# Optimization experiments

Hardware: AMD Instinct MI355X
Metric: run time of the kernel (lower is better)

## Reference

```python
import jax, jax.numpy as jnp
import numpy as np

V = 100000   # nodes
E = 1600000  # edges (avg degree 16)
LN = 64      # feat_dim
S = 8        # stat_dim
T = 4        # recurrence steps
MU = 0.9
N_EDGE_TYPES = 10


def _uniform_linear(kw, kb, fan_out, fan_in):
    # torch nn.Linear default init: U(-1/sqrt(fan_in), 1/sqrt(fan_in))
    lim = 1.0 / np.sqrt(fan_in)
    W = jax.random.uniform(kw, (fan_out, fan_in), jnp.float32, -lim, lim)
    b = jax.random.uniform(kb, (fan_out,), jnp.float32, -lim, lim)
    return W, b


def setup_inputs() -> dict:
    key = jax.random.key(0)
    ks = jax.random.split(key, 12)
    feat_Matrix = jax.random.normal(ks[0], (V, LN), jnp.float32)
    X_Node = jax.random.randint(ks[1], (E,), 1, V + 1, dtype=jnp.int64)   # 1-indexed
    X_Neis = jax.random.randint(ks[2], (E,), 1, V + 1, dtype=jnp.int64)   # 1-indexed
    edge_type_index = jax.random.randint(ks[3], (E,), 1, N_EDGE_TYPES + 1, dtype=jnp.int32)
    dg_list = jax.random.randint(ks[4], (E,), 1, 65).astype(jnp.float32)  # degrees >= 1
    H_init = jax.random.uniform(ks[5], (V, S), jnp.float32)  # torch.rand init of state
    W_xi, b_xi = _uniform_linear(ks[6], ks[7], S * S, 2 * LN + N_EDGE_TYPES)
    W_rou, b_rou = _uniform_linear(ks[8], ks[9], S, LN)
    W1, b1 = _uniform_linear(ks[10], ks[11], 1, S)
    return {
        "feat_Matrix": feat_Matrix, "X_Node": X_Node, "X_Neis": X_Neis,
        "edge_type_index": edge_type_index, "dg_list": dg_list, "H_init": H_init,
        "W_xi": W_xi, "b_xi": b_xi, "W_rou": W_rou, "b_rou": b_rou,
        "W1": W1, "b1": b1,
    }


def reference(feat_Matrix, X_Node, X_Neis, edge_type_index, dg_list, H_init,
              W_xi, b_xi, W_rou, b_rou, W1, b1):
    src = X_Node - 1           # 0-indexed source nodes
    dst = X_Neis - 1           # 0-indexed neighbor nodes (for embedding gather)
    node_emb = feat_Matrix[src]            # [E, LN]
    neis_emb = feat_Matrix[dst]            # [E, LN]
    et = jax.nn.one_hot(edge_type_index - 1, N_EDGE_TYPES, dtype=jnp.float32)
    X = jnp.concatenate([node_emb, neis_emb, et], axis=1)  # [E, 2*LN+10]

    # Xi(X): per-edge transition matrices A, constant across steps -> precompute
    A = jnp.tanh(X @ W_xi.T + b_xi).reshape(-1, S, S)
    A = A * (MU / S) / dg_list[:, None, None]              # [E, S, S]
    # Rou(neis_emb): per-edge bias b, constant across steps
    bias = jnp.tanh(neis_emb @ W_rou.T + b_rou)            # [E, S]

    def step(H, _):
        He = H[src]                                        # gather [E, S]
        out = jnp.einsum('eij,ej->ei', A, He) + bias       # per-edge small matmul
        # AggrSum: dense one-hot mask vs RAW 1-indexed X_Neis against range(0,V-1)
        # -> scatter by 1-indexed ids; ids == V fall out of range and are dropped.
        Hn = jax.ops.segment_sum(out, X_Neis, num_segments=V)
        return Hn, None

    H, _ = jax.lax.scan(step, H_init, None, length=T)      # [V, S]

    logits = (H @ W1.T + b1).squeeze(-1)                   # [V]
    attn = jax.nn.softmax(logits)                          # softmax over nodes
    graph_out = jnp.tanh(jnp.sum(H * attn[:, None], axis=0))  # [S]
    return graph_out
```

## Files before the change

### kernel.cpp

```cpp
#include <hip/hip_runtime.h>
#include <hip/hip_bf16.h>

constexpr int V   = 100000;
constexpr int E   = 1600000;
constexpr int NET = 10;
constexpr int KXW = 138;
constexpr int NB  = (V + 255) / 256;
constexpr int GN  = 8;
constexpr int NEB = E / 256;
constexpr int NPQ = (V / 16 + 3) / 4;
constexpr float MUS   = 0.1125f;
constexpr float SP    = 0.025f;
constexpr float LOG2E = 1.44269504f;
constexpr float S2L   = 2.0f * SP * LOG2E;
constexpr float K7    = MUS / 7.0f;

typedef __attribute__((ext_vector_type(8))) short short8;
typedef __attribute__((ext_vector_type(4))) float float4v;

__device__ __forceinline__ float fast_tanh(float x) {
    return 1.0f - 2.0f * __builtin_amdgcn_rcpf(__expf(2.0f * x) + 1.0f);
}
__device__ __forceinline__ float bflo(unsigned u) { return __uint_as_float(u << 16); }
__device__ __forceinline__ float bfhi(unsigned u) { return __uint_as_float(u & 0xffff0000u); }
__device__ __forceinline__ short f2bf(float x) {
    union { __hip_bfloat16 b; short s; } u; u.b = __float2bfloat16(x); return u.s;
}

__device__ __forceinline__ float ub0(unsigned u) {
#if __has_builtin(__builtin_amdgcn_cvt_f32_ubyte0)
    return __builtin_amdgcn_cvt_f32_ubyte0(u);
#else
    return (float)(u & 0xff);
#endif
}
__device__ __forceinline__ float ub1(unsigned u) {
#if __has_builtin(__builtin_amdgcn_cvt_f32_ubyte1)
    return __builtin_amdgcn_cvt_f32_ubyte1(u);
#else
    return (float)((u >> 8) & 0xff);
#endif
}
__device__ __forceinline__ float ub2(unsigned u) {
#if __has_builtin(__builtin_amdgcn_cvt_f32_ubyte2)
    return __builtin_amdgcn_cvt_f32_ubyte2(u);
#else
    return (float)((u >> 16) & 0xff);
#endif
}
__device__ __forceinline__ float ub3(unsigned u) {
#if __has_builtin(__builtin_amdgcn_cvt_f32_ubyte3)
    return __builtin_amdgcn_cvt_f32_ubyte3(u);
#else
    return (float)(u >> 24);
#endif
}

__device__ __forceinline__ int dot8i4(unsigned a, unsigned b, int c) {
#if __has_builtin(__builtin_amdgcn_sdot8)
    return __builtin_amdgcn_sdot8((int)a, (int)b, c, false);
#else
    int r = c;
    #pragma unroll
    for (int j = 0; j < 8; ++j) {
        int av = ((int)(a << (28 - 4 * j))) >> 28;
        int bv = ((int)(b << (28 - 4 * j))) >> 28;
        r += av * bv;
    }
    return r;
#endif
}

__global__ __launch_bounds__(256) void histg_pq_kernel(
    const int* __restrict__ xneis, int* __restrict__ countg,
    int* __restrict__ rank0,
    const float* __restrict__ feat, const float* __restrict__ Wxi,
    unsigned char* __restrict__ P8, ushort* __restrict__ Qb)
{
    if (blockIdx.x < NEB) {
        int e = blockIdx.x * 256 + threadIdx.x;
        int g = blockIdx.x & (GN - 1);
        int nr = xneis[e];
        if (nr < V) rank0[e] = atomicAdd(&countg[g * V + nr], 1);
        return;
    }
    int bid = blockIdx.x - NEB;
    const int lane = threadIdx.x & 63, wave = threadIdx.x >> 6;
    const int quad = lane >> 4, l16 = lane & 15;

    short8 bP[4][2], bQ[4][2];
    #pragma unroll
    for (int nt = 0; nt < 4; ++nt) {
        #pragma unroll
        for (int ks = 0; ks < 2; ++ks) {
            const float* wp = Wxi + (size_t)(nt * 16 + l16) * KXW + ks * 32 + quad * 8;
            short8 p, q;
            #pragma unroll
            for (int j = 0; j < 8; ++j) { p[j] = f2bf(wp[j]); q[j] = f2bf(wp[64 + j]); }
            bP[nt][ks] = p; bQ[nt][ks] = q;
        }
    }

    int t = bid * 4 + wave;
    if (t >= V / 16) return;
    int v0 = t * 16;

    const float* fp = feat + (size_t)(v0 + l16) * 64 + quad * 8;
    short8 a0, a1;
    #pragma unroll
    for (int j = 0; j < 8; ++j) { a0[j] = f2bf(fp[j]); a1[j] = f2bf(fp[32 + j]); }

    float4v accP[4], accQ[4];
    #pragma unroll
    for (int nt = 0; nt < 4; ++nt) {
        float4v z = {0.f, 0.f, 0.f, 0.f};
        z = __builtin_amdgcn_mfma_f32_16x16x32_bf16(a0, bP[nt][0], z, 0, 0, 0);
        z = __builtin_amdgcn_mfma_f32_16x16x32_bf16(a1, bP[nt][1], z, 0, 0, 0);
        accP[nt] = z;
        float4v w = {0.f, 0.f, 0.f, 0.f};
        w = __builtin_amdgcn_mfma_f32_16x16x32_bf16(a0, bQ[nt][0], w, 0, 0, 0);
        w = __builtin_amdgcn_mfma_f32_16x16x32_bf16(a1, bQ[nt][1], w, 0, 0, 0);
        accQ[nt] = w;
    }

    #pragma unroll
    for (int r = 0; r < 4; ++r) {
        int row = v0 + quad * 4 + r;
        #pragma unroll
        for (int nt = 0; nt < 4; ++nt) {
            int col = nt * 16 + l16;
            int q8 = (int)rintf(accP[nt][r] * (1.0f / SP)) + 128;
            q8 = min(max(q8, 0), 255);
            P8[row * 64 + col] = (unsigned char)q8;
            Qb[row * 64 + col] = (ushort)f2bf(accQ[nt][r]);
        }
    }
}

__global__ __launch_bounds__(256) void scanV_bsum_kernel(
    const int* __restrict__ countg, int* __restrict__ offg,
    int* __restrict__ scanned, int* __restrict__ bsumT,
    const float* __restrict__ feat, const float* __restrict__ Wrou,
    const float* __restrict__ brou, const float* __restrict__ Hinit,
    float* __restrict__ Bsum, uint2* __restrict__ Hq0)
{
    __shared__ int s[256];
    __shared__ float Wl[512];
    __shared__ float bl[8];
    int tid = threadIdx.x;
    for (int i = tid; i < 512; i += 256) Wl[i] = Wrou[i];
    if (tid < 8) bl[tid] = brou[tid];

    int v = blockIdx.x * 256 + tid;
    int c = 0;
    if (v < V) {
        int run = 0;
        #pragma unroll
        for (int g = 0; g < GN; ++g) {
            offg[g * V + v] = run;
            run += countg[g * V + v];
        }
        c = run;
    }
    s[tid] = c; __syncthreads();
    #pragma unroll
    for (int off = 1; off < 256; off <<= 1) {
        int t = (tid >= off) ? s[tid - off] : 0;
        __syncthreads();
        s[tid] += t;
        __syncthreads();
    }
    if (v < V) scanned[v] = s[tid] - c;
    if (tid == 255) bsumT[blockIdx.x] = s[255];

    if (v >= V) return;
    float out[8] = {0, 0, 0, 0, 0, 0, 0, 0};
    if (c > 0) {
        const float4* f4 = (const float4*)(feat + (size_t)(v - 1) * 64);
        float acc[8];
        #pragma unroll
        for (int ss = 0; ss < 8; ++ss) acc[ss] = bl[ss];
        #pragma unroll 4
        for (int k = 0; k < 16; ++k) {
            float4 x = f4[k];
            #pragma unroll
            for (int ss = 0; ss < 8; ++ss) {
                const float* w = &Wl[ss * 64 + k * 4];
                acc[ss] += x.x * w[0] + x.y * w[1] + x.z * w[2] + x.w * w[3];
            }
        }
        float fc = (float)c;
        #pragma unroll
        for (int ss = 0; ss < 8; ++ss) out[ss] = fc * fast_tanh(acc[ss]);
    }
    float4* O = (float4*)(Bsum + (size_t)v * 8);
    O[0] = make_float4(out[0], out[1], out[2], out[3]);
    O[1] = make_float4(out[4], out[5], out[6], out[7]);

    const float4* Hh4 = (const float4*)(Hinit + (size_t)v * 8);
    float4 h0 = Hh4[0], h1 = Hh4[1];
    float hv[8] = {h0.x, h0.y, h0.z, h0.w, h1.x, h1.y, h1.z, h1.w};
    float mx = 0.0f;
    #pragma unroll
    for (int i = 0; i < 8; ++i) mx = fmaxf(mx, fabsf(hv[i]));
    float si = (mx > 0.0f) ? 7.0f / mx : 0.0f;
    unsigned w = 0;
    #pragma unroll
    for (int i = 0; i < 8; ++i)
        w |= ((unsigned)((int)rintf(hv[i] * si)) & 0xFu) << (4 * i);
    Hq0[v] = make_uint2(w, __float_as_uint(mx * (1.0f / 7.0f)));
}

__global__ __launch_bounds__(512) void scan_tops_kernel(
    const int* __restrict__ blocksum, int* __restrict__ tops, int* __restrict__ rowptr)
{
    __shared__ int s[512];
    int tid = threadIdx.x;
    int v = (tid < NB) ? blocksum[tid] : 0;
    s[tid] = v; __syncthreads();
    #pragma unroll
    for (int off = 1; off < 512; off <<= 1) {
        int t = (tid >= off) ? s[tid - off] : 0;
        __syncthreads();
        s[tid] += t;
        __syncthreads();
    }
    if (tid < NB) tops[tid] = s[tid] - v;
    if (tid == 511) rowptr[V] = s[511];
}

__global__ __launch_bounds__(256) void add_offsets_kernel(
    const int* __restrict__ scanned, const int* __restrict__ tops, int* __restrict__ rowptr)
{
    int i = blockIdx.x * 256 + threadIdx.x;
    if (i < V) rowptr[i] = scanned[i] + tops[blockIdx.x];
}

__global__ __launch_bounds__(256) void scatterA_kernel(
    const int* __restrict__ xnode, const int* __restrict__ xneis,
    const int* __restrict__ etype, const float* __restrict__ dg,
    const int* __restrict__ rowptr, const int* __restrict__ offg,
    const int* __restrict__ rank0, uint2* __restrict__ buc,
    int* __restrict__ bcnt)
{
    __shared__ int wcnt[4][8];
    __shared__ int woff[4][8];
    int tid = threadIdx.x;
    int lane = tid & 63, wv = tid >> 6;
    int e = blockIdx.x * 256 + tid;
    int g = blockIdx.x & (GN - 1);

    int nr = xneis[e];
    bool keep = (nr < V);
    int p = -1, r = 0;
    if (keep) {
        p = rowptr[nr] + offg[g * V + nr] + rank0[e];
        r = p >> 18;
    }

    unsigned rnk = 0;
    #pragma unroll
    for (int r8 = 0; r8 < 8; ++r8) {
        unsigned long long m = __ballot(keep && (r == r8));
        if (keep && r == r8)
            rnk = (unsigned)__popcll(m & ((1ull << lane) - 1ull));
        if (lane == 0) wcnt[wv][r8] = (int)__popcll(m);
    }
    __syncthreads();
    if (tid < 8) {
        int run = 0;
        #pragma unroll
        for (int w = 0; w < 4; ++w) { woff[w][tid] = run; run += wcnt[w][tid]; }
        bcnt[blockIdx.x * 8 + tid] = run;
    }
    __syncthreads();

    if (keep) {
        unsigned src = (unsigned)(xnode[e] - 1);
        unsigned et  = (unsigned)(etype[e] - 1);
        unsigned dgi = (unsigned)dg[e] - 1;
        unsigned meta = src | (et << 17) | (dgi << 21);
        int slot = blockIdx.x * 2048 + r * 256 + woff[wv][r] + (int)rnk;
        buc[slot] = make_uint2((unsigned)p, meta);
    }
}

__global__ __launch_bounds__(256) void drain_kernel(
    const uint2* __restrict__ buc, const int* __restrict__ bcnt,
    unsigned* __restrict__ pmeta)
{
    int r = blockIdx.x & 7;
    int nstride = (int)(gridDim.x >> 3);
    for (int sb = (int)(blockIdx.x >> 3); sb < NEB; sb += nstride) {
        int c = bcnt[sb * 8 + r];
        const uint2* seg = buc + (size_t)sb * 2048 + r * 256;
        for (int i = threadIdx.x; i < c; i += 256) {
            uint2 t = seg[i];
            pmeta[t.x] = t.y;
        }
    }
}

__global__ __launch_bounds__(256) void amat_kernel(
    const unsigned* __restrict__ pmeta, const int* __restrict__ rowptr,
    const unsigned char* __restrict__ P8, const ushort* __restrict__ Qb,
    const float* __restrict__ Wxi, const float* __restrict__ bxi,
    const uint2* __restrict__ Hq0, const float* __restrict__ Bsum,
    unsigned* __restrict__ A4, uint2* __restrict__ HqOut)
{
    __shared__ float Wet2[NET * 64];
    int tid = threadIdx.x;
    for (int i = tid; i < NET * 64; i += 256) {
        int et = i >> 6, n = i & 63;
        Wet2[i] = 2.0f * LOG2E * (Wxi[n * KXW + 128 + et] + bxi[n]);
    }
    __syncthreads();

    int v = blockIdx.x * 4 + (tid >> 6);
    if (v >= V) return;
    int lane = tid & 63;
    int el = lane >> 3, s = lane & 7;

    const int off = rowptr[v];
    const int deg = rowptr[v + 1] - off;

    float q0, q1, q2, q3, q4, q5, q6, q7;
    {
        uint4 qu = *(const uint4*)(Qb + v * 64 + s * 8);
        const float B = 128.0f * SP, C = 2.0f * LOG2E;
        q0 = C * (bflo(qu.x) - B); q1 = C * (bfhi(qu.x) - B);
        q2 = C * (bflo(qu.y) - B); q3 = C * (bfhi(qu.y) - B);
        q4 = C * (bflo(qu.z) - B); q5 = C * (bfhi(qu.z) - B);
        q6 = C * (bflo(qu.w) - B); q7 = C * (bfhi(qu.w) - B);
    }

    float accD = 0.0f;

    for (int base = 0; base < deg; base += 64) {
        unsigned m_mine = 0;
        {
            int i1 = base + lane;
            if (i1 < deg) m_mine = pmeta[off + i1];
        }
        int nb = deg - base;
        for (int k = 0; k * 8 + el < nb && k < 8; ++k) {
            int ib = k * 8 + el;
            int i = base + ib;
            unsigned m = __shfl(m_mine, ib);
            int src = (int)(m & 0x1FFFF);
            int et  = (int)((m >> 17) & 0xF);

            uint2 pu = *(const uint2*)(P8 + src * 64 + s * 8);
            const float4* w4 = (const float4*)(&Wet2[et * 64 + s * 8]);
            float4 wa = w4[0], wb = w4[1];
            uint2 hq = Hq0[src];

            float r0 = __builtin_amdgcn_rcpf(__builtin_amdgcn_exp2f(fmaf(ub0(pu.x), S2L, q0 + wa.x)) + 1.0f);
            float r1 = __builtin_amdgcn_rcpf(__builtin_amdgcn_exp2f(fmaf(ub1(pu.x), S2L, q1 + wa.y)) + 1.0f);
            float r2 = __builtin_amdgcn_rcpf(__builtin_amdgcn_exp2f(fmaf(ub2(pu.x), S2L, q2 + wa.z)) + 1.0f);
            float r3 = __builtin_amdgcn_rcpf(__builtin_amdgcn_exp2f(fmaf(ub3(pu.x), S2L, q3 + wa.w)) + 1.0f);
            float r4 = __builtin_amdgcn_rcpf(__builtin_amdgcn_exp2f(fmaf(ub0(pu.y), S2L, q4 + wb.x)) + 1.0f);
            float r5 = __builtin_amdgcn_rcpf(__builtin_amdgcn_exp2f(fmaf(ub1(pu.y), S2L, q5 + wb.y)) + 1.0f);
            float r6 = __builtin_amdgcn_rcpf(__builtin_amdgcn_exp2f(fmaf(ub2(pu.y), S2L, q6 + wb.z)) + 1.0f);
            float r7 = __builtin_amdgcn_rcpf(__builtin_amdgcn_exp2f(fmaf(ub3(pu.y), S2L, q7 + wb.w)) + 1.0f);

            int n0 = (int)rintf(fmaf(r0, -14.0f, 7.0f));
            int n1 = (int)rintf(fmaf(r1, -14.0f, 7.0f));
            int n2 = (int)rintf(fmaf(r2, -14.0f, 7.0f));
            int n3 = (int)rintf(fmaf(r3, -14.0f, 7.0f));
            int n4 = (int)rintf(fmaf(r4, -14.0f, 7.0f));
            int n5 = (int)rintf(fmaf(r5, -14.0f, 7.0f));
            int n6 = (int)rintf(fmaf(r6, -14.0f, 7.0f));
            int n7 = (int)rintf(fmaf(r7, -14.0f, 7.0f));

            unsigned w = ((unsigned)n0 & 0xFu)        | (((unsigned)n1 & 0xFu) << 4)
                       | (((unsigned)n2 & 0xFu) << 8)  | (((unsigned)n3 & 0xFu) << 12)
                       | (((unsigned)n4 & 0xFu) << 16) | (((unsigned)n5 & 0xFu) << 20)
                       | (((unsigned)n6 & 0xFu) << 24) | (((unsigned)n7 & 0xFu) << 28);
            A4[(unsigned)(off + i) * 8u + (unsigned)s] = w;

            int dd = dot8i4(w, hq.x, 0);
            float rdg = __builtin_amdgcn_rcpf((float)((int)(m >> 21) + 1));
            accD = fmaf((float)dd, __uint_as_float(hq.y) * rdg, accD);
        }
    }
    accD += __shfl_xor(accD, 8);  accD += __shfl_xor(accD, 16); accD += __shfl_xor(accD, 32);
    float h1v = accD * K7 + Bsum[v * 8 + s];

    float mx = fabsf(h1v);
    mx = fmaxf(mx, __shfl_xor(mx, 1));
    mx = fmaxf(mx, __shfl_xor(mx, 2));
    mx = fmaxf(mx, __shfl_xor(mx, 4));
    float si = (mx > 0.0f) ? 7.0f / mx : 0.0f;
    unsigned nib = (unsigned)((int)rintf(h1v * si)) & 0xFu;
    unsigned b1 = __shfl(nib, lane + 1), b2 = __shfl(nib, lane + 2), b3 = __shfl(nib, lane + 3);
    unsigned b4 = __shfl(nib, lane + 4), b5 = __shfl(nib, lane + 5);
    unsigned b6 = __shfl(nib, lane + 6), b7 = __shfl(nib, lane + 7);
    if (lane == 0) {
        unsigned w = nib | (b1 << 4) | (b2 << 8) | (b3 << 12)
                   | (b4 << 16) | (b5 << 20) | (b6 << 24) | (b7 << 28);
        HqOut[v] = make_uint2(w, __float_as_uint(mx * (1.0f / 7.0f)));
    }
}

__global__ __launch_bounds__(256) void step_kernel(
    const uint2* __restrict__ HqIn, uint2* __restrict__ HqOut,
    const unsigned* __restrict__ pmeta, const int* __restrict__ rowptr,
    const unsigned* __restrict__ A4, const float* __restrict__ Bsum,
    const float* __restrict__ W1, const float* __restrict__ b1,
    float* __restrict__ logitsOut, float* __restrict__ HfpOut)
{
    int v = blockIdx.x * 64 + (threadIdx.x >> 2);
    if (v >= V) return;
    int q = threadIdx.x & 3;

    int p0 = rowptr[v], p1 = rowptr[v + 1];

    float aE0 = 0.f, aO0 = 0.f, aE1 = 0.f, aO1 = 0.f;
    float aE2 = 0.f, aO2 = 0.f, aE3 = 0.f, aO3 = 0.f;
    int p = p0;
    for (; p + 3 < p1; p += 4) {
        unsigned m0 = pmeta[p],     m1 = pmeta[p + 1];
        unsigned m2 = pmeta[p + 2], m3 = pmeta[p + 3];
        uint2 au0 = *(const uint2*)(A4 + (unsigned)p * 8u + (unsigned)(q * 2));
        uint2 au1 = *(const uint2*)(A4 + (unsigned)(p + 1) * 8u + (unsigned)(q * 2));
        uint2 au2 = *(const uint2*)(A4 + (unsigned)(p + 2) * 8u + (unsigned)(q * 2));
        uint2 au3 = *(const uint2*)(A4 + (unsigned)(p + 3) * 8u + (unsigned)(q * 2));
        uint2 hq0 = HqIn[m0 & 0x1FFFFu];
        uint2 hq1 = HqIn[m1 & 0x1FFFFu];
        uint2 hq2 = HqIn[m2 & 0x1FFFFu];
        uint2 hq3 = HqIn[m3 & 0x1FFFFu];

        float sc0 = __uint_as_float(hq0.y) * __builtin_amdgcn_rcpf((float)((int)(m0 >> 21) + 1));
        aE0 = fmaf((float)dot8i4(au0.x, hq0.x, 0), sc0, aE0);
        aO0 = fmaf((float)dot8i4(au0.y, hq0.x, 0), sc0, aO0);
        float sc1 = __uint_as_float(hq1.y) * __builtin_amdgcn_rcpf((float)((int)(m1 >> 21) + 1));
        aE1 = fmaf((float)dot8i4(au1.x, hq1.x, 0), sc1, aE1);
        aO1 = fmaf((float)dot8i4(au1.y, hq1.x, 0), sc1, aO1);
        float sc2 = __uint_as_float(hq2.y) * __builtin_amdgcn_rcpf((float)((int)(m2 >> 21) + 1));
        aE2 = fmaf((float)dot8i4(au2.x, hq2.x, 0), sc2, aE2);
        aO2 = fmaf((float)dot8i4(au2.y, hq2.x, 0), sc2, aO2);
        float sc3 = __uint_as_float(hq3.y) * __builtin_amdgcn_rcpf((float)((int)(m3 >> 21) + 1));
        aE3 = fmaf((float)dot8i4(au3.x, hq3.x, 0), sc3, aE3);
        aO3 = fmaf((float)dot8i4(au3.y, hq3.x, 0), sc3, aO3);
    }
    for (; p + 1 < p1; p += 2) {
        unsigned m0 = pmeta[p], m1 = pmeta[p + 1];
        uint2 au0 = *(const uint2*)(A4 + (unsigned)p * 8u + (unsigned)(q * 2));
        uint2 au1 = *(const uint2*)(A4 + (unsigned)(p + 1) * 8u + (unsigned)(q * 2));
        uint2 hq0 = HqIn[m0 & 0x1FFFFu];
        uint2 hq1 = HqIn[m1 & 0x1FFFFu];
        float sc0 = __uint_as_float(hq0.y) * __builtin_amdgcn_rcpf((float)((int)(m0 >> 21) + 1));
        aE0 = fmaf((float)dot8i4(au0.x, hq0.x, 0), sc0, aE0);
        aO0 = fmaf((float)dot8i4(au0.y, hq0.x, 0), sc0, aO0);
        float sc1 = __uint_as_float(hq1.y) * __builtin_amdgcn_rcpf((float)((int)(m1 >> 21) + 1));
        aE1 = fmaf((float)dot8i4(au1.x, hq1.x, 0), sc1, aE1);
        aO1 = fmaf((float)dot8i4(au1.y, hq1.x, 0), sc1, aO1);
    }
    if (p < p1) {
        unsigned m = pmeta[p];
        uint2 au = *(const uint2*)(A4 + (unsigned)p * 8u + (unsigned)(q * 2));
        uint2 hq = HqIn[m & 0x1FFFFu];
        float sc = __uint_as_float(hq.y) * __builtin_amdgcn_rcpf((float)((int)(m >> 21) + 1));
        aE0 = fmaf((float)dot8i4(au.x, hq.x, 0), sc, aE0);
        aO0 = fmaf((float)dot8i4(au.y, hq.x, 0), sc, aO0);
    }
    float accE = (aE0 + aE1) + (aE2 + aE3);
    float accO = (aO0 + aO1) + (aO2 + aO3);

    float2 bs = *(const float2*)(Bsum + v * 8 + q * 2);
    float hE = accE * K7 + bs.x;
    float hO = accO * K7 + bs.y;

    float mx = fmaxf(fabsf(hE), fabsf(hO));
    mx = fmaxf(mx, __shfl_xor(mx, 1));
    mx = fmaxf(mx, __shfl_xor(mx, 2));
    float si = (mx > 0.0f) ? 7.0f / mx : 0.0f;
    unsigned nE = (unsigned)((int)rintf(hE * si)) & 0xFu;
    unsigned nO = (unsigned)((int)rintf(hO * si)) & 0xFu;
    unsigned wq = (nE | (nO << 4)) << (8 * q);
    wq |= __shfl_xor(wq, 1);
    wq |= __shfl_xor(wq, 2);
    if (q == 0)
        HqOut[v] = make_uint2(wq, __float_as_uint(mx * (1.0f / 7.0f)));
    if (HfpOut != nullptr)
        *(float2*)(HfpOut + v * 8 + q * 2) = make_float2(hE, hO);
    if (logitsOut != nullptr) {
        float t = hE * W1[q * 2] + hO * W1[q * 2 + 1];
        t += __shfl_xor(t, 1); t += __shfl_xor(t, 2);
        if (q == 0) logitsOut[v] = t + b1[0];
    }
}

__global__ __launch_bounds__(256) void sum_kernel(
    const float* __restrict__ H, const float* __restrict__ logits,
    float* __restrict__ partial)
{
    float m = -INFINITY, se = 0.0f;
    float sh[8] = {0, 0, 0, 0, 0, 0, 0, 0};
    for (int v = blockIdx.x * 256 + threadIdx.x; v < V; v += 64 * 256) {
        float l = logits[v];
        float mn = fmaxf(m, l);
        float a = __expf(m - mn);
        float w = __expf(l - mn);
        se = se * a + w;
        const float4* H4 = (const float4*)(H + (size_t)v * 8);
        float4 h0 = H4[0], h1 = H4[1];
        sh[0] = sh[0] * a + w * h0.x; sh[1] = sh[1] * a + w * h0.y;
        sh[2] = sh[2] * a + w * h0.z; sh[3] = sh[3] * a + w * h0.w;
        sh[4] = sh[4] * a + w * h1.x; sh[5] = sh[5] * a + w * h1.y;
        sh[6] = sh[6] * a + w * h1.z; sh[7] = sh[7] * a + w * h1.w;
        m = mn;
    }
    #pragma unroll
    for (int o = 1; o < 64; o <<= 1) {
        float mo = __shfl_xor(m, o), seo = __shfl_xor(se, o);
        float sho[8];
        #pragma unroll
        for (int i = 0; i < 8; ++i) sho[i] = __shfl_xor(sh[i], o);
        float mn = fmaxf(m, mo);
        float a = __expf(m - mn), b = __expf(mo - mn);
        se = se * a + seo * b;
        #pragma unroll
        for (int i = 0; i < 8; ++i) sh[i] = sh[i] * a + sho[i] * b;
        m = mn;
    }
    __shared__ float sm[4][10];
    int wv = threadIdx.x >> 6;
    if ((threadIdx.x & 63) == 0) {
        sm[wv][0] = m; sm[wv][9] = se;
        #pragma unroll
        for (int i = 0; i < 8; ++i) sm[wv][1 + i] = sh[i];
    }
    __syncthreads();
    if (threadIdx.x == 0) {
        float M = sm[0][0], SE = 0.0f, SH[8] = {0, 0, 0, 0, 0, 0, 0, 0};
        #pragma unroll
        for (int w2 = 1; w2 < 4; ++w2) M = fmaxf(M, sm[w2][0]);
        #pragma unroll
        for (int w2 = 0; w2 < 4; ++w2) {
            float a = __expf(sm[w2][0] - M);
            SE += sm[w2][9] * a;
            #pragma unroll
            for (int i = 0; i < 8; ++i) SH[i] += sm[w2][1 + i] * a;
        }
        partial[blockIdx.x * 12 + 0] = M;
        partial[blockIdx.x * 12 + 9] = SE;
        #pragma unroll
        for (int i = 0; i < 8; ++i) partial[blockIdx.x * 12 + 1 + i] = SH[i];
    }
}

__global__ void final_kernel(const float* __restrict__ partial, float* __restrict__ out)
{
    int lane = threadIdx.x;
    float m = partial[lane * 12 + 0];
    float se = partial[lane * 12 + 9];
    float sh[8];
    #pragma unroll
    for (int i = 0; i < 8; ++i) sh[i] = partial[lane * 12 + 1 + i];
    #pragma unroll
    for (int o = 1; o < 64; o <<= 1) {
        float mo = __shfl_xor(m, o), seo = __shfl_xor(se, o);
        float sho[8];
        #pragma unroll
        for (int i = 0; i < 8; ++i) sho[i] = __shfl_xor(sh[i], o);
        float mn = fmaxf(m, mo);
        float a = __expf(m - mn), b = __expf(mo - mn);
        se = se * a + seo * b;
        #pragma unroll
        for (int i = 0; i < 8; ++i) sh[i] = sh[i] * a + sho[i] * b;
        m = mn;
    }
    if (lane < 8) out[lane] = tanhf(sh[lane] / se);
}

extern "C" void kernel_launch(void* const* d_in, const int* in_sizes, int n_in,
                              void* d_out, int out_size, void* d_ws, size_t ws_size,
                              hipStream_t stream)
{
    const float* feat  = (const float*)d_in[0];
    const int*   xnode = (const int*)d_in[1];
    const int*   xneis = (const int*)d_in[2];
    const int*   etype = (const int*)d_in[3];
    const float* dg    = (const float*)d_in[4];
    const float* Hinit = (const float*)d_in[5];
    const float* Wxi   = (const float*)d_in[6];
    const float* bxi   = (const float*)d_in[7];
    const float* Wrou  = (const float*)d_in[8];
    const float* brou  = (const float*)d_in[9];
    const float* W1    = (const float*)d_in[10];
    const float* b1    = (const float*)d_in[11];

    char* ws = (char*)d_ws;
    auto alloc = [&](size_t bytes) -> char* {
        char* p = ws; ws += (bytes + 255) & ~(size_t)255; return p;
    };
    unsigned* A4      = (unsigned*)alloc((size_t)E * 32);
    uint2*    buc     = (uint2*)alloc((size_t)NEB * 2048 * 8);
    unsigned char* P8 = (unsigned char*)alloc((size_t)V * 64);
    ushort*   Qb      = (ushort*)alloc((size_t)V * 64 * 2);
    unsigned* pmeta   = (unsigned*)alloc((size_t)E * 4);
    int*      rank0   = (int*)alloc((size_t)E * 4);
    int*      countg  = (int*)alloc((size_t)GN * V * 4);
    int*      offg    = (int*)alloc((size_t)GN * V * 4);
    int*      bcnt    = (int*)alloc((size_t)NEB * 8 * 4);
    int*      scanned = (int*)alloc((size_t)V * 4);
    int*      rowptr  = (int*)alloc((size_t)(V + 1) * 4);
    int*      bsumT   = (int*)alloc(512 * 4);
    int*      topsT   = (int*)alloc(512 * 4);
    uint2*    Hq0     = (uint2*)alloc((size_t)V * 8);
    uint2*    HqA     = (uint2*)alloc((size_t)V * 8);
    uint2*    HqB     = (uint2*)alloc((size_t)V * 8);
    float*    Hfp     = (float*)alloc((size_t)V * 8 * 4);
    float*    Bsum    = (float*)alloc((size_t)V * 8 * 4);
    float*    logits  = (float*)alloc((size_t)V * 4);
    float*    spart   = (float*)alloc(64 * 12 * 4);

    hipMemsetAsync(countg, 0, (size_t)GN * V * 4, stream);
    histg_pq_kernel<<<NEB + NPQ, 256, 0, stream>>>(xneis, countg, rank0,
                                                   feat, Wxi, P8, Qb);
    scanV_bsum_kernel<<<NB, 256, 0, stream>>>(countg, offg, scanned, bsumT,
                                              feat, Wrou, brou, Hinit,
                                              Bsum, Hq0);
    scan_tops_kernel<<<1, 512, 0, stream>>>(bsumT, topsT, rowptr);
    add_offsets_kernel<<<NB, 256, 0, stream>>>(scanned, topsT, rowptr);
    scatterA_kernel<<<NEB, 256, 0, stream>>>(xnode, xneis, etype, dg,
                                             rowptr, offg, rank0, buc, bcnt);
    drain_kernel<<<2048, 256, 0, stream>>>(buc, bcnt, pmeta);
    amat_kernel<<<(V + 3) / 4, 256, 0, stream>>>(pmeta, rowptr, P8, Qb, Wxi, bxi,
                                                 Hq0, Bsum, A4, HqA);

    const uint2* Hcur = HqA;
    uint2* bufs[2] = {HqB, HqA};
    for (int t = 0; t < 3; ++t) {
        uint2* Hn = bufs[t & 1];
        float* lg  = (t == 2) ? logits : nullptr;
        float* hf  = (t == 2) ? Hfp : nullptr;
        step_kernel<<<(V + 63) / 64, 256, 0, stream>>>(Hcur, Hn, pmeta, rowptr,
                                                       A4, Bsum, W1, b1, lg, hf);
        Hcur = Hn;
    }

    sum_kernel<<<64, 256, 0, stream>>>(Hfp, logits, spart);
    final_kernel<<<1, 64, 0, stream>>>(spart, (float*)d_out);
}
```

Baseline: 394.9 us.

## Move Rou bias and H quantization into histogram kernel; merge scan-tops with offsets

Moves the per-node Rou tanh computation and the H_init 4-bit quantization out of the scan kernel into extra blocks of the first histogram/P-Q kernel, so they overlap with the atomic histogram work. The scan kernel now only multiplies the stored tanh values by the count. The single-block top scan and the add-offsets kernel are merged into one kernel where every block redoes the small 391-entry scan, removing a launch. The cost is an extra V*8 float intermediate buffer and redundant scans per block.

```diff
diff --git a/kernel.cpp b/kernel.cpp
--- a/kernel.cpp
+++ b/kernel.cpp
@@ -71,11 +71,14 @@
 #endif
 }
 
-__global__ __launch_bounds__(256) void histg_pq_kernel(
+__global__ __launch_bounds__(256) void shadow_kernel(
     const int* __restrict__ xneis, int* __restrict__ countg,
     int* __restrict__ rank0,
     const float* __restrict__ feat, const float* __restrict__ Wxi,
-    unsigned char* __restrict__ P8, ushort* __restrict__ Qb)
+    unsigned char* __restrict__ P8, ushort* __restrict__ Qb,
+    const float* __restrict__ Wrou, const float* __restrict__ brou,
+    const float* __restrict__ Hinit, float* __restrict__ T8,
+    uint2* __restrict__ Hq0)
 {
     if (blockIdx.x < NEB) {
         int e = blockIdx.x * 256 + threadIdx.x;
@@ -84,73 +87,115 @@
         if (nr < V) rank0[e] = atomicAdd(&countg[g * V + nr], 1);
         return;
     }
-    int bid = blockIdx.x - NEB;
-    const int lane = threadIdx.x & 63, wave = threadIdx.x >> 6;
-    const int quad = lane >> 4, l16 = lane & 15;
-
-    short8 bP[4][2], bQ[4][2];
-    #pragma unroll
-    for (int nt = 0; nt < 4; ++nt) {
-        #pragma unroll
-        for (int ks = 0; ks < 2; ++ks) {
-            const float* wp = Wxi + (size_t)(nt * 16 + l16) * KXW + ks * 32 + quad * 8;
-            short8 p, q;
+    if (blockIdx.x < NEB + NPQ) {
+        int bid = blockIdx.x - NEB;
+        const int lane = threadIdx.x & 63, wave = threadIdx.x >> 6;
+        const int quad = lane >> 4, l16 = lane & 15;
+
+        short8 bP[4][2], bQ[4][2];
+        #pragma unroll
+        for (int nt = 0; nt < 4; ++nt) {
             #pragma unroll
-            for (int j = 0; j < 8; ++j) { p[j] = f2bf(wp[j]); q[j] = f2bf(wp[64 + j]); }
-            bP[nt][ks] = p; bQ[nt][ks] = q;
-        }
-    }
-
-    int t = bid * 4 + wave;
-    if (t >= V / 16) return;
-    int v0 = t * 16;
-
-    const float* fp = feat + (size_t)(v0 + l16) * 64 + quad * 8;
-    short8 a0, a1;
-    #pragma unroll
-    for (int j = 0; j < 8; ++j) { a0[j] = f2bf(fp[j]); a1[j] = f2bf(fp[32 + j]); }
-
-    float4v accP[4], accQ[4];
-    #pragma unroll
-    for (int nt = 0; nt < 4; ++nt) {
-        float4v z = {0.f, 0.f, 0.f, 0.f};
-        z = __builtin_amdgcn_mfma_f32_16x16x32_bf16(a0, bP[nt][0], z, 0, 0, 0);
-        z = __builtin_amdgcn_mfma_f32_16x16x32_bf16(a1, bP[nt][1], z, 0, 0, 0);
-        accP[nt] = z;
-        float4v w = {0.f, 0.f, 0.f, 0.f};
-        w = __builtin_amdgcn_mfma_f32_16x16x32_bf16(a0, bQ[nt][0], w, 0, 0, 0);
-        w = __builtin_amdgcn_mfma_f32_16x16x32_bf16(a1, bQ[nt][1], w, 0, 0, 0);
-        accQ[nt] = w;
-    }
-
-    #pragma unroll
-    for (int r = 0; r < 4; ++r) {
-        int row = v0 + quad * 4 + r;
+            for (int ks = 0; ks < 2; ++ks) {
+                const float* wp = Wxi + (size_t)(nt * 16 + l16) * KXW + ks * 32 + quad * 8;
+                short8 p, q;
+                #pragma unroll
+                for (int j = 0; j < 8; ++j) { p[j] = f2bf(wp[j]); q[j] = f2bf(wp[64 + j]); }
+                bP[nt][ks] = p; bQ[nt][ks] = q;
+            }
+        }
+
+        int t = bid * 4 + wave;
+        if (t >= V / 16) return;
+        int v0 = t * 16;
+
+        const float* fp = feat + (size_t)(v0 + l16) * 64 + quad * 8;
+        short8 a0, a1;
+        #pragma unroll
+        for (int j = 0; j < 8; ++j) { a0[j] = f2bf(fp[j]); a1[j] = f2bf(fp[32 + j]); }
+
+        float4v accP[4], accQ[4];
         #pragma unroll
         for (int nt = 0; nt < 4; ++nt) {
-            int col = nt * 16 + l16;
-            int q8 = (int)rintf(accP[nt][r] * (1.0f / SP)) + 128;
-            q8 = min(max(q8, 0), 255);
-            P8[row * 64 + col] = (unsigned char)q8;
-            Qb[row * 64 + col] = (ushort)f2bf(accQ[nt][r]);
-        }
-    }
-}
-
-__global__ __launch_bounds__(256) void scanV_bsum_kernel(
+            float4v z = {0.f, 0.f, 0.f, 0.f};
+            z = __builtin_amdgcn_mfma_f32_16x16x32_bf16(a0, bP[nt][0], z, 0, 0, 0);
+            z = __builtin_amdgcn_mfma_f32_16x16x32_bf16(a1, bP[nt][1], z, 0, 0, 0);
+            accP[nt] = z;
+            float4v w = {0.f, 0.f, 0.f, 0.f};
+            w = __builtin_amdgcn_mfma_f32_16x16x32_bf16(a0, bQ[nt][0], w, 0, 0, 0);
+            w = __builtin_amdgcn_mfma_f32_16x16x32_bf16(a1, bQ[nt][1], w, 0, 0, 0);
+            accQ[nt] = w;
+        }
+
+        #pragma unroll
+        for (int r = 0; r < 4; ++r) {
+            int row = v0 + quad * 4 + r;
+            #pragma unroll
+            for (int nt = 0; nt < 4; ++nt) {
+                int col = nt * 16 + l16;
+                int q8 = (int)rintf(accP[nt][r] * (1.0f / SP)) + 128;
+                q8 = min(max(q8, 0), 255);
+                P8[row * 64 + col] = (unsigned char)q8;
+                Qb[row * 64 + col] = (ushort)f2bf(accQ[nt][r]);
+            }
+        }
+        return;
+    }
+    {
+        __shared__ float Wl[512];
+        __shared__ float bl[8];
+        int tid = threadIdx.x;
+        for (int i = tid; i < 512; i += 256) Wl[i] = Wrou[i];
+        if (tid < 8) bl[tid] = brou[tid];
+        __syncthreads();
+
+        int v = (blockIdx.x - NEB - NPQ) * 256 + tid;
+        if (v >= V) return;
+
+        float out[8] = {0, 0, 0, 0, 0, 0, 0, 0};
+        if (v >= 1) {
+            const float4* f4 = (const float4*)(feat + (size_t)(v - 1) * 64);
+            float acc[8];
+            #pragma unroll
+            for (int ss = 0; ss < 8; ++ss) acc[ss] = bl[ss];
+            #pragma unroll 4
+            for (int k = 0; k < 16; ++k) {
+                float4 x = f4[k];
+                #pragma unroll
+                for (int ss = 0; ss < 8; ++ss) {
+                    const float* w = &Wl[ss * 64 + k * 4];
+                    acc[ss] += x.x * w[0] + x.y * w[1] + x.z * w[2] + x.w * w[3];
+                }
+            }
+            #pragma unroll
+            for (int ss = 0; ss < 8; ++ss) out[ss] = fast_tanh(acc[ss]);
+        }
+        float4* O = (float4*)(T8 + (size_t)v * 8);
+        O[0] = make_float4(out[0], out[1], out[2], out[3]);
+        O[1] = make_float4(out[4], out[5], out[6], out[7]);
+
+        const float4* Hh4 = (const float4*)(Hinit + (size_t)v * 8);
+        float4 h0 = Hh4[0], h1 = Hh4[1];
+        float hv[8] = {h0.x, h0.y, h0.z, h0.w, h1.x, h1.y, h1.z, h1.w};
+        float mx = 0.0f;
+        #pragma unroll
+        for (int i = 0; i < 8; ++i) mx = fmaxf(mx, fabsf(hv[i]));
+        float si = (mx > 0.0f) ? 7.0f / mx : 0.0f;
+        unsigned w = 0;
+        #pragma unroll
+        for (int i = 0; i < 8; ++i)
+            w |= ((unsigned)((int)rintf(hv[i] * si)) & 0xFu) << (4 * i);
+        Hq0[v] = make_uint2(w, __float_as_uint(mx * (1.0f / 7.0f)));
+    }
+}
+
+__global__ __launch_bounds__(256) void scanV_kernel(
     const int* __restrict__ countg, int* __restrict__ offg,
     int* __restrict__ scanned, int* __restrict__ bsumT,
-    const float* __restrict__ feat, const float* __restrict__ Wrou,
-    const float* __restrict__ brou, const float* __restrict__ Hinit,
-    float* __restrict__ Bsum, uint2* __restrict__ Hq0)
+    const float* __restrict__ T8, float* __restrict__ Bsum)
 {
     __shared__ int s[256];
-    __shared__ float Wl[512];
-    __shared__ float bl[8];
     int tid = threadIdx.x;
-    for (int i = tid; i < 512; i += 256) Wl[i] = Wrou[i];
-    if (tid < 8) bl[tid] = brou[tid];
-
     int v = blockIdx.x * 256 + tid;
     int c = 0;
     if (v < V) {
@@ -173,51 +218,25 @@
     if (v < V) scanned[v] = s[tid] - c;
     if (tid == 255) bsumT[blockIdx.x] = s[255];
 
-    if (v >= V) return;
-    float out[8] = {0, 0, 0, 0, 0, 0, 0, 0};
-    if (c > 0) {
-        const float4* f4 = (const float4*)(feat + (size_t)(v - 1) * 64);
-        float acc[8];
-        #pragma unroll
-        for (int ss = 0; ss < 8; ++ss) acc[ss] = bl[ss];
-        #pragma unroll 4
-        for (int k = 0; k < 16; ++k) {
-            float4 x = f4[k];
-            #pragma unroll
-            for (int ss = 0; ss < 8; ++ss) {
-                const float* w = &Wl[ss * 64 + k * 4];
-                acc[ss] += x.x * w[0] + x.y * w[1] + x.z * w[2] + x.w * w[3];
-            }
-        }
+    if (v < V) {
         float fc = (float)c;
-        #pragma unroll
-        for (int ss = 0; ss < 8; ++ss) out[ss] = fc * fast_tanh(acc[ss]);
-    }
-    float4* O = (float4*)(Bsum + (size_t)v * 8);
-    O[0] = make_float4(out[0], out[1], out[2], out[3]);
-    O[1] = make_float4(out[4], out[5], out[6], out[7]);
-
-    const float4* Hh4 = (const float4*)(Hinit + (size_t)v * 8);
-    float4 h0 = Hh4[0], h1 = Hh4[1];
-    float hv[8] = {h0.x, h0.y, h0.z, h0.w, h1.x, h1.y, h1.z, h1.w};
-    float mx = 0.0f;
-    #pragma unroll
-    for (int i = 0; i < 8; ++i) mx = fmaxf(mx, fabsf(hv[i]));
-    float si = (mx > 0.0f) ? 7.0f / mx : 0.0f;
-    unsigned w = 0;
-    #pragma unroll
-    for (int i = 0; i < 8; ++i)
-        w |= ((unsigned)((int)rintf(hv[i] * si)) & 0xFu) << (4 * i);
-    Hq0[v] = make_uint2(w, __float_as_uint(mx * (1.0f / 7.0f)));
-}
-
-__global__ __launch_bounds__(512) void scan_tops_kernel(
-    const int* __restrict__ blocksum, int* __restrict__ tops, int* __restrict__ rowptr)
+        const float4* T4 = (const float4*)(T8 + (size_t)v * 8);
+        float4 t0 = T4[0], t1 = T4[1];
+        float4* O = (float4*)(Bsum + (size_t)v * 8);
+        O[0] = make_float4(fc * t0.x, fc * t0.y, fc * t0.z, fc * t0.w);
+        O[1] = make_float4(fc * t1.x, fc * t1.y, fc * t1.z, fc * t1.w);
+    }
+}
+
+__global__ __launch_bounds__(512) void rowptr_kernel(
+    const int* __restrict__ bsumT, const int* __restrict__ scanned,
+    int* __restrict__ rowptr)
 {
     __shared__ int s[512];
+    __shared__ int tot;
     int tid = threadIdx.x;
-    int v = (tid < NB) ? blocksum[tid] : 0;
-    s[tid] = v; __syncthreads();
+    int val = (tid < NB) ? bsumT[tid] : 0;
+    s[tid] = val; __syncthreads();
     #pragma unroll
     for (int off = 1; off < 512; off <<= 1) {
         int t = (tid >= off) ? s[tid - off] : 0;
@@ -225,15 +244,14 @@
         s[tid] += t;
         __syncthreads();
     }
-    if (tid < NB) tops[tid] = s[tid] - v;
-    if (tid == 511) rowptr[V] = s[511];
-}
-
-__global__ __launch_bounds__(256) void add_offsets_kernel(
-    const int* __restrict__ scanned, const int* __restrict__ tops, int* __restrict__ rowptr)
-{
-    int i = blockIdx.x * 256 + threadIdx.x;
-    if (i < V) rowptr[i] = scanned[i] + tops[blockIdx.x];
+    if (tid == NB - 1) tot = s[tid];
+    __syncthreads();
+    int top = s[blockIdx.x] - bsumT[blockIdx.x];
+    if (tid < 256) {
+        int i = blockIdx.x * 256 + tid;
+        if (i < V) rowptr[i] = scanned[i] + top;
+    }
+    if (blockIdx.x == 0 && tid == 0) rowptr[V] = tot;
 }
 
 __global__ __launch_bounds__(256) void scatterA_kernel(
@@ -608,7 +626,7 @@
     int*      scanned = (int*)alloc((size_t)V * 4);
     int*      rowptr  = (int*)alloc((size_t)(V + 1) * 4);
     int*      bsumT   = (int*)alloc(512 * 4);
-    int*      topsT   = (int*)alloc(512 * 4);
+    float*    T8      = (float*)alloc((size_t)V * 8 * 4);
     uint2*    Hq0     = (uint2*)alloc((size_t)V * 8);
     uint2*    HqA     = (uint2*)alloc((size_t)V * 8);
     uint2*    HqB     = (uint2*)alloc((size_t)V * 8);
@@ -618,13 +636,11 @@
     float*    spart   = (float*)alloc(64 * 12 * 4);
 
     hipMemsetAsync(countg, 0, (size_t)GN * V * 4, stream);
-    histg_pq_kernel<<<NEB + NPQ, 256, 0, stream>>>(xneis, countg, rank0,
-                                                   feat, Wxi, P8, Qb);
-    scanV_bsum_kernel<<<NB, 256, 0, stream>>>(countg, offg, scanned, bsumT,
-                                              feat, Wrou, brou, Hinit,
-                                              Bsum, Hq0);
-    scan_tops_kernel<<<1, 512, 0, stream>>>(bsumT, topsT, rowptr);
-    add_offsets_kernel<<<NB, 256, 0, stream>>>(scanned, topsT, rowptr);
+    shadow_kernel<<<NEB + NPQ + NB, 256, 0, stream>>>(
+        xneis, countg, rank0, feat, Wxi, P8, Qb,
+        Wrou, brou, Hinit, T8, Hq0);
+    scanV_kernel<<<NB, 256, 0, stream>>>(countg, offg, scanned, bsumT, T8, Bsum);
+    rowptr_kernel<<<NB, 512, 0, stream>>>(bsumT, scanned, rowptr);
     scatterA_kernel<<<NEB, 256, 0, stream>>>(xnode, xneis, etype, dg,
                                              rowptr, offg, rank0, buc, bcnt);
     drain_kernel<<<2048, 256, 0, stream>>>(buc, bcnt, pmeta);
```

Result: no change. 389.4 us (-1.4%).
